# Performance work log

Measured on AMD Instinct MI355X. Metric: run time of the kernel, lower is better.

Reference implementation:

```python
import jax, jax.numpy as jnp
import numpy as np

N = 8192
IN_F = 512
OUT_F = 256
EDGE_P = 0.02  # adjacency density


def setup_inputs() -> dict:
    key = jax.random.key(0)
    k1, k2, k3, k4 = jax.random.split(key, 4)
    x = jax.random.normal(k1, (N, IN_F), dtype=jnp.float32)
    # xavier_uniform with gain=1.414 ~ std gain*sqrt(2/(fan_in+fan_out))
    W = jax.random.normal(k2, (IN_F, OUT_F), dtype=jnp.float32) * (1.414 * np.sqrt(2.0 / (IN_F + OUT_F)))
    a = jax.random.normal(k3, (2 * OUT_F, 1), dtype=jnp.float32) * (1.414 * np.sqrt(2.0 / (2 * OUT_F + 1)))
    adj = (jax.random.uniform(k4, (N, N)) < EDGE_P).astype(jnp.float32)
    return {"x": x, "adj": adj, "W": W, "a": a}


def reference(x, adj, W, a):
    h = x @ W                        # [N, F]
    F = h.shape[1]
    # repeat/cat reduces to an outer sum of two [N] vectors.
    s_src = (h @ a[:F]).squeeze(-1)  # [N], contribution of h_i
    s_dst = (h @ a[F:]).squeeze(-1)  # [N], contribution of h_j
    e = jax.nn.leaky_relu(s_src[:, None] + s_dst[None, :], negative_slope=0.2)  # [N, N]
    # NOTE: original code softmaxes over the FULL row, THEN multiplies by adj.
    attention = jax.nn.softmax(e, axis=1) * adj  # [N, N]
    h_prime = attention @ h                      # [N, F]
    return h_prime, attention
```

## Files before the change

kernel.cpp:

```cpp
#include <hip/hip_runtime.h>
#include <hip/hip_bf16.h>

#define N_NODES 8192
#define IN_F    512
#define OUT_F   256
#define K1_ROWS 16
#define MAXNZ   512

typedef float v4f __attribute__((ext_vector_type(4)));

__global__ __launch_bounds__(256) void k_gemm_h(const float* __restrict__ x,
                                                const float* __restrict__ W,
                                                float* __restrict__ h) {
  __shared__ float xs[K1_ROWS][IN_F];
  const int t  = threadIdx.x;
  const int r0 = blockIdx.x * K1_ROWS;

  const float4* xg  = (const float4*)(x + (size_t)r0 * IN_F);
  float4*       xls = (float4*)&xs[0][0];
#pragma unroll
  for (int c = 0; c < 8; ++c) xls[c * 256 + t] = xg[c * 256 + t];
  __syncthreads();

  float acc[K1_ROWS];
#pragma unroll
  for (int r = 0; r < K1_ROWS; ++r) acc[r] = 0.f;

  for (int k = 0; k < IN_F; k += 4) {
    const float w0 = W[(k + 0) * OUT_F + t];
    const float w1 = W[(k + 1) * OUT_F + t];
    const float w2 = W[(k + 2) * OUT_F + t];
    const float w3 = W[(k + 3) * OUT_F + t];
#pragma unroll
    for (int r = 0; r < K1_ROWS; ++r) {
      const float4 xv = *(const float4*)&xs[r][k];
      acc[r] = fmaf(xv.x, w0, acc[r]);
      acc[r] = fmaf(xv.y, w1, acc[r]);
      acc[r] = fmaf(xv.z, w2, acc[r]);
      acc[r] = fmaf(xv.w, w3, acc[r]);
    }
  }
#pragma unroll
  for (int r = 0; r < K1_ROWS; ++r) h[(size_t)(r0 + r) * OUT_F + t] = acc[r];
}

__global__ __launch_bounds__(256) void k_scores(const float* __restrict__ h,
                                                const float* __restrict__ a,
                                                float* __restrict__ s_src,
                                                float* __restrict__ s_dst) {
  const int row = blockIdx.x * 4 + (threadIdx.x >> 6);
  const int l   = threadIdx.x & 63;
  const float4 hv = ((const float4*)(h + (size_t)row * OUT_F))[l];
  const float4 a0 = ((const float4*)a)[l];
  const float4 a1 = ((const float4*)(a + OUT_F))[l];
  float p0 = hv.x * a0.x + hv.y * a0.y + hv.z * a0.z + hv.w * a0.w;
  float p1 = hv.x * a1.x + hv.y * a1.y + hv.z * a1.z + hv.w * a1.w;
#pragma unroll
  for (int off = 32; off > 0; off >>= 1) {
    p0 += __shfl_down(p0, off);
    p1 += __shfl_down(p1, off);
  }
  if (l == 0) { s_src[row] = p0; s_dst[row] = p1; }
}

__device__ __forceinline__ float lrelu_exp(float v) {
  const float e = v > 0.f ? v : 0.2f * v;
  return __expf(e);
}

__global__ __launch_bounds__(256) void k_attn(const float* __restrict__ adj,
                                              const float* __restrict__ h,
                                              const float* __restrict__ s_src,
                                              const float* __restrict__ s_dst,
                                              float* __restrict__ out_hp,
                                              float* __restrict__ out_att) {
  __shared__ float nza[MAXNZ];
  __shared__ int   nzj[MAXNZ];
  __shared__ float redbuf[4];
  __shared__ int   cnt;

  const int t = threadIdx.x;
  const int i = blockIdx.x;
  const float ssrc = s_src[i];
  if (t == 0) cnt = 0;

  const float4* sd4 = (const float4*)s_dst;

  float lsum = 0.f;
#pragma unroll
  for (int c = 0; c < N_NODES / 1024; ++c) {
    const float4 s = sd4[c * 256 + t];
    lsum += lrelu_exp(ssrc + s.x);
    lsum += lrelu_exp(ssrc + s.y);
    lsum += lrelu_exp(ssrc + s.z);
    lsum += lrelu_exp(ssrc + s.w);
  }
#pragma unroll
  for (int off = 32; off > 0; off >>= 1) lsum += __shfl_down(lsum, off);
  if ((t & 63) == 0) redbuf[t >> 6] = lsum;
  __syncthreads();
  const float inv = 1.0f / (redbuf[0] + redbuf[1] + redbuf[2] + redbuf[3]);

  const v4f* adj4 = (const v4f*)(adj + (size_t)i * N_NODES);
  v4f*       att4 = (v4f*)(out_att + (size_t)i * N_NODES);
#pragma unroll 2
  for (int c = 0; c < N_NODES / 1024; ++c) {
    const int j4 = c * 256 + t;
    const v4f av = __builtin_nontemporal_load(adj4 + j4);
    const float4 s = sd4[j4];
    v4f att;
    att.x = av.x * lrelu_exp(ssrc + s.x) * inv;
    att.y = av.y * lrelu_exp(ssrc + s.y) * inv;
    att.z = av.z * lrelu_exp(ssrc + s.z) * inv;
    att.w = av.w * lrelu_exp(ssrc + s.w) * inv;
    __builtin_nontemporal_store(att, att4 + j4);
    const int j = j4 * 4;
    if (av.x != 0.f) { const int k = atomicAdd(&cnt, 1); if (k < MAXNZ) { nzj[k] = j + 0; nza[k] = att.x; } }
    if (av.y != 0.f) { const int k = atomicAdd(&cnt, 1); if (k < MAXNZ) { nzj[k] = j + 1; nza[k] = att.y; } }
    if (av.z != 0.f) { const int k = atomicAdd(&cnt, 1); if (k < MAXNZ) { nzj[k] = j + 2; nza[k] = att.z; } }
    if (av.w != 0.f) { const int k = atomicAdd(&cnt, 1); if (k < MAXNZ) { nzj[k] = j + 3; nza[k] = att.w; } }
  }
  __syncthreads();

  const int n = cnt < MAXNZ ? cnt : MAXNZ;
  float acc = 0.f;
#pragma unroll 4
  for (int k = 0; k < n; ++k) {
    acc = fmaf(nza[k], h[(size_t)nzj[k] * OUT_F + t], acc);
  }
  out_hp[(size_t)i * OUT_F + t] = acc;
}

extern "C" void kernel_launch(void* const* d_in, const int* in_sizes, int n_in,
                              void* d_out, int out_size, void* d_ws, size_t ws_size,
                              hipStream_t stream) {
  const float* x   = (const float*)d_in[0];
  const float* adj = (const float*)d_in[1];
  const float* W   = (const float*)d_in[2];
  const float* a   = (const float*)d_in[3];

  float* out_hp  = (float*)d_out;
  float* out_att = (float*)d_out + (size_t)N_NODES * OUT_F;

  float* h_ws    = (float*)d_ws;
  float* ssrc_ws = h_ws + (size_t)N_NODES * OUT_F;
  float* sdst_ws = ssrc_ws + N_NODES;

  k_gemm_h<<<N_NODES / K1_ROWS, 256, 0, stream>>>(x, W, h_ws);
  k_scores<<<N_NODES / 4, 256, 0, stream>>>(h_ws, a, ssrc_ws, sdst_ws);
  k_attn<<<N_NODES, 256, 0, stream>>>(adj, h_ws, ssrc_ws, sdst_ws, out_hp, out_att);
}
```

Measured before the change: 597.1 us.

## Register-tile the feature GEMM and batch adjacency loads in attention kernel

Replaces the row-block feature GEMM with a 64x64x32 shared-memory tiled GEMM in which each thread computes a 4x4 register tile, raising arithmetic intensity and cutting repeated global reads of W. In the attention kernel, the s_dst values are loaded once into registers and reused for both the softmax sum and the output pass, and all eight adjacency vectors per thread are issued before any compute to increase memory-level parallelism. The gather loop unroll grows from 4 to 8. In exchange, register pressure rises, which may lower occupancy in the bandwidth-bound attention kernel.

```diff
diff --git a/kernel.cpp b/kernel.cpp
--- a/kernel.cpp
+++ b/kernel.cpp
@@ -4,44 +4,74 @@
 #define N_NODES 8192
 #define IN_F    512
 #define OUT_F   256
-#define K1_ROWS 16
 #define MAXNZ   512
+
+#define BM 64
+#define BN 64
+#define BK 32
 
 typedef float v4f __attribute__((ext_vector_type(4)));
 
 __global__ __launch_bounds__(256) void k_gemm_h(const float* __restrict__ x,
                                                 const float* __restrict__ W,
                                                 float* __restrict__ h) {
-  __shared__ float xs[K1_ROWS][IN_F];
+  __shared__ float As[BK][BM + 4];
+  __shared__ float Bs[BK][BN];
   const int t  = threadIdx.x;
-  const int r0 = blockIdx.x * K1_ROWS;
+  const int bm = blockIdx.x >> 2;
+  const int bn = blockIdx.x & 3;
+  const int m0 = bm * BM, n0 = bn * BN;
+  const int tm = (t >> 4) * 4;
+  const int tn = (t & 15) * 4;
 
-  const float4* xg  = (const float4*)(x + (size_t)r0 * IN_F);
-  float4*       xls = (float4*)&xs[0][0];
+  float acc[4][4] = {{0.f, 0.f, 0.f, 0.f}, {0.f, 0.f, 0.f, 0.f},
+                     {0.f, 0.f, 0.f, 0.f}, {0.f, 0.f, 0.f, 0.f}};
+
+  for (int k0 = 0; k0 < IN_F; k0 += BK) {
 #pragma unroll
-  for (int c = 0; c < 8; ++c) xls[c * 256 + t] = xg[c * 256 + t];
-  __syncthreads();
-
-  float acc[K1_ROWS];
+    for (int i = 0; i < 2; ++i) {
+      const int fi = t + i * 256;
+      const int ar = fi >> 3;
+      const int ac = (fi & 7) << 2;
+      const float4 va = *(const float4*)&x[(size_t)(m0 + ar) * IN_F + k0 + ac];
+      As[ac + 0][ar] = va.x;
+      As[ac + 1][ar] = va.y;
+      As[ac + 2][ar] = va.z;
+      As[ac + 3][ar] = va.w;
+      const int br = fi >> 4;
+      const int bc = (fi & 15) << 2;
+      *(float4*)&Bs[br][bc] = *(const float4*)&W[(size_t)(k0 + br) * OUT_F + n0 + bc];
+    }
+    __syncthreads();
 #pragma unroll
-  for (int r = 0; r < K1_ROWS; ++r) acc[r] = 0.f;
-
-  for (int k = 0; k < IN_F; k += 4) {
-    const float w0 = W[(k + 0) * OUT_F + t];
-    const float w1 = W[(k + 1) * OUT_F + t];
-    const float w2 = W[(k + 2) * OUT_F + t];
-    const float w3 = W[(k + 3) * OUT_F + t];
-#pragma unroll
-    for (int r = 0; r < K1_ROWS; ++r) {
-      const float4 xv = *(const float4*)&xs[r][k];
-      acc[r] = fmaf(xv.x, w0, acc[r]);
-      acc[r] = fmaf(xv.y, w1, acc[r]);
-      acc[r] = fmaf(xv.z, w2, acc[r]);
-      acc[r] = fmaf(xv.w, w3, acc[r]);
+    for (int k = 0; k < BK; ++k) {
+      const float4 a = *(const float4*)&As[k][tm];
+      const float4 b = *(const float4*)&Bs[k][tn];
+      acc[0][0] = fmaf(a.x, b.x, acc[0][0]);
+      acc[0][1] = fmaf(a.x, b.y, acc[0][1]);
+      acc[0][2] = fmaf(a.x, b.z, acc[0][2]);
+      acc[0][3] = fmaf(a.x, b.w, acc[0][3]);
+      acc[1][0] = fmaf(a.y, b.x, acc[1][0]);
+      acc[1][1] = fmaf(a.y, b.y, acc[1][1]);
+      acc[1][2] = fmaf(a.y, b.z, acc[1][2]);
+      acc[1][3] = fmaf(a.y, b.w, acc[1][3]);
+      acc[2][0] = fmaf(a.z, b.x, acc[2][0]);
+      acc[2][1] = fmaf(a.z, b.y, acc[2][1]);
+      acc[2][2] = fmaf(a.z, b.z, acc[2][2]);
+      acc[2][3] = fmaf(a.z, b.w, acc[2][3]);
+      acc[3][0] = fmaf(a.w, b.x, acc[3][0]);
+      acc[3][1] = fmaf(a.w, b.y, acc[3][1]);
+      acc[3][2] = fmaf(a.w, b.z, acc[3][2]);
+      acc[3][3] = fmaf(a.w, b.w, acc[3][3]);
     }
+    __syncthreads();
   }
 #pragma unroll
-  for (int r = 0; r < K1_ROWS; ++r) h[(size_t)(r0 + r) * OUT_F + t] = acc[r];
+  for (int r = 0; r < 4; ++r) {
+    float4 o;
+    o.x = acc[r][0]; o.y = acc[r][1]; o.z = acc[r][2]; o.w = acc[r][3];
+    *(float4*)&h[(size_t)(m0 + tm + r) * OUT_F + n0 + tn] = o;
+  }
 }
 
 __global__ __launch_bounds__(256) void k_scores(const float* __restrict__ h,
@@ -85,15 +115,15 @@
   if (t == 0) cnt = 0;
 
   const float4* sd4 = (const float4*)s_dst;
+  float4 sd[8];
+#pragma unroll
+  for (int c = 0; c < 8; ++c) sd[c] = sd4[c * 256 + t];
 
   float lsum = 0.f;
 #pragma unroll
-  for (int c = 0; c < N_NODES / 1024; ++c) {
-    const float4 s = sd4[c * 256 + t];
-    lsum += lrelu_exp(ssrc + s.x);
-    lsum += lrelu_exp(ssrc + s.y);
-    lsum += lrelu_exp(ssrc + s.z);
-    lsum += lrelu_exp(ssrc + s.w);
+  for (int c = 0; c < 8; ++c) {
+    lsum += lrelu_exp(ssrc + sd[c].x) + lrelu_exp(ssrc + sd[c].y)
+          + lrelu_exp(ssrc + sd[c].z) + lrelu_exp(ssrc + sd[c].w);
   }
 #pragma unroll
   for (int off = 32; off > 0; off >>= 1) lsum += __shfl_down(lsum, off);
@@ -103,28 +133,28 @@
 
   const v4f* adj4 = (const v4f*)(adj + (size_t)i * N_NODES);
   v4f*       att4 = (v4f*)(out_att + (size_t)i * N_NODES);
-#pragma unroll 2
-  for (int c = 0; c < N_NODES / 1024; ++c) {
-    const int j4 = c * 256 + t;
-    const v4f av = __builtin_nontemporal_load(adj4 + j4);
-    const float4 s = sd4[j4];
+  v4f av[8];
+#pragma unroll
+  for (int c = 0; c < 8; ++c) av[c] = __builtin_nontemporal_load(adj4 + c * 256 + t);
+#pragma unroll
+  for (int c = 0; c < 8; ++c) {
     v4f att;
-    att.x = av.x * lrelu_exp(ssrc + s.x) * inv;
-    att.y = av.y * lrelu_exp(ssrc + s.y) * inv;
-    att.z = av.z * lrelu_exp(ssrc + s.z) * inv;
-    att.w = av.w * lrelu_exp(ssrc + s.w) * inv;
-    __builtin_nontemporal_store(att, att4 + j4);
-    const int j = j4 * 4;
-    if (av.x != 0.f) { const int k = atomicAdd(&cnt, 1); if (k < MAXNZ) { nzj[k] = j + 0; nza[k] = att.x; } }
-    if (av.y != 0.f) { const int k = atomicAdd(&cnt, 1); if (k < MAXNZ) { nzj[k] = j + 1; nza[k] = att.y; } }
-    if (av.z != 0.f) { const int k = atomicAdd(&cnt, 1); if (k < MAXNZ) { nzj[k] = j + 2; nza[k] = att.z; } }
-    if (av.w != 0.f) { const int k = atomicAdd(&cnt, 1); if (k < MAXNZ) { nzj[k] = j + 3; nza[k] = att.w; } }
+    att.x = av[c].x * (lrelu_exp(ssrc + sd[c].x) * inv);
+    att.y = av[c].y * (lrelu_exp(ssrc + sd[c].y) * inv);
+    att.z = av[c].z * (lrelu_exp(ssrc + sd[c].z) * inv);
+    att.w = av[c].w * (lrelu_exp(ssrc + sd[c].w) * inv);
+    __builtin_nontemporal_store(att, att4 + c * 256 + t);
+    const int j = (c * 256 + t) * 4;
+    if (av[c].x != 0.f) { const int k = atomicAdd(&cnt, 1); if (k < MAXNZ) { nzj[k] = j + 0; nza[k] = att.x; } }
+    if (av[c].y != 0.f) { const int k = atomicAdd(&cnt, 1); if (k < MAXNZ) { nzj[k] = j + 1; nza[k] = att.y; } }
+    if (av[c].z != 0.f) { const int k = atomicAdd(&cnt, 1); if (k < MAXNZ) { nzj[k] = j + 2; nza[k] = att.z; } }
+    if (av[c].w != 0.f) { const int k = atomicAdd(&cnt, 1); if (k < MAXNZ) { nzj[k] = j + 3; nza[k] = att.w; } }
   }
   __syncthreads();
 
   const int n = cnt < MAXNZ ? cnt : MAXNZ;
   float acc = 0.f;
-#pragma unroll 4
+#pragma unroll 8
   for (int k = 0; k < n; ++k) {
     acc = fmaf(nza[k], h[(size_t)nzj[k] * OUT_F + t], acc);
   }
@@ -146,7 +176,7 @@
   float* ssrc_ws = h_ws + (size_t)N_NODES * OUT_F;
   float* sdst_ws = ssrc_ws + N_NODES;
 
-  k_gemm_h<<<N_NODES / K1_ROWS, 256, 0, stream>>>(x, W, h_ws);
+  k_gemm_h<<<(N_NODES / BM) * (OUT_F / BN), 256, 0, stream>>>(x, W, h_ws);
   k_scores<<<N_NODES / 4, 256, 0, stream>>>(h_ws, a, ssrc_ws, sdst_ws);
   k_attn<<<N_NODES, 256, 0, stream>>>(adj, h_ws, ssrc_ws, sdst_ws, out_hp, out_att);
 }
```

New measurement: 541.9 us. 9.3% less time.
